# Optimization experiments

Hardware: AMD Instinct MI355X
Metric: run time of the kernel (lower is better)

Reference implementation:

```python
import jax, jax.numpy as jnp
import numpy as np

HEADS = 8
DIM_HEAD = 64
DIM = 256
INNER = HEADS * DIM_HEAD  # 512


def setup_inputs() -> dict:
    key = jax.random.key(0)
    ks = jax.random.split(key, 5)
    b_times_r, n = 32, 1024
    x = jax.random.normal(ks[0], (b_times_r, n, DIM), dtype=jnp.float32)
    # nn.Linear weights stored as (in, out) so y = x @ W
    Wq = jax.random.normal(ks[1], (DIM, INNER), dtype=jnp.float32) * 0.02
    Wkv = jax.random.normal(ks[2], (DIM, 2 * INNER), dtype=jnp.float32) * 0.02
    Wout = jax.random.normal(ks[3], (INNER, DIM), dtype=jnp.float32) * 0.02
    bout = jax.random.normal(ks[4], (DIM,), dtype=jnp.float32) * 0.02
    return {"x": x, "Wq": Wq, "Wkv": Wkv, "Wout": Wout, "bout": bout, "tie_attn_dim": 32}


def reference(x, Wq, Wkv, Wout, bout, tie_attn_dim):
    r = tie_attn_dim
    br, n, _ = x.shape
    b = br // r
    q = x @ Wq                                   # (b*r, n, inner)
    k, v = jnp.split(x @ Wkv, 2, axis=-1)        # (b*r, n, inner) each

    def split_heads(t):
        # (b*r) n (h d) -> b r h n d
        return t.reshape(b, r, n, HEADS, DIM_HEAD).transpose(0, 1, 3, 2, 4)

    q, k, v = map(split_heads, (q, k, v))
    scale = (DIM_HEAD ** -0.5) * (r ** -0.5)
    # tied attention: sum logits over the MSA row dim r
    dots = jnp.einsum('brhid,brhjd->bhij', q, k) * scale  # (b, h, n, n)
    attn = jax.nn.softmax(dots, axis=-1)
    out = jnp.einsum('bhij,brhjd->brhid', attn, v)        # (b, r, h, n, d)
    out = out.transpose(0, 1, 3, 2, 4).reshape(br, n, INNER)
    return out @ Wout + bout
```

## Files before the change

kernel.cpp:

```cpp
#include <hip/hip_runtime.h>
#include <math.h>

typedef unsigned short bf16u;
typedef __attribute__((ext_vector_type(8))) short short8;
typedef __attribute__((ext_vector_type(4))) float f32x4;

__device__ __forceinline__ bf16u f2bf(float f) {
    unsigned int u = __float_as_uint(f);
    u += 0x7fffu + ((u >> 16) & 1u);
    return (bf16u)(u >> 16);
}
__device__ __forceinline__ float bf2f(bf16u h) {
    return __uint_as_float(((unsigned int)h) << 16);
}

__device__ __forceinline__ void gload16(const void* g, void* s) {
    __builtin_amdgcn_global_load_lds((const __attribute__((address_space(1))) void*)g,
                                     (__attribute__((address_space(3))) void*)s, 16, 0, 0);
}

#define MM(a_, b_, c_) c_ = __builtin_amdgcn_mfma_f32_16x16x32_bf16(a_, b_, c_, 0, 0, 0)
#define BAR() __builtin_amdgcn_s_barrier()

#define STG() do { if (q < nht) { \
    const int t_ = q >> 2, p_ = q & 3; \
    const bf16u* P_ = (p_ < 2) ? B : A; \
    const long s_ = ((p_ < 2) ? brow : arow) + ((p_ & 1) ? r128 : 0) + t_ * 64; \
    bf16u* d_ = S + ((t_ & 1) << 15) + ((p_ < 2) ? 16384 : 0) + ((p_ & 1) << 12) + (w << 9); \
    gload16(P_ + s_, d_); \
    gload16(P_ + s_ + 32, d_ + 8192); \
  } ++q; } while (0)

#define RDA(dst, t, m, kk) dst = *(const short8*)(S + (((t) & 1) << 15) + ((kk) << 13) + ((wr * 8 + (m)) << 9) + (l << 3))
#define RDB(dst, t, n, kk) dst = *(const short8*)(S + (((t) & 1) << 15) + 16384 + ((kk) << 13) + ((wc * 4 + (n)) << 9) + (l << 3))

#define KTILE(t, VMASM) do { \
  RDA(af[0][0],t,0,0); RDA(af[0][1],t,0,1); RDA(af[1][0],t,1,0); RDA(af[1][1],t,1,1); \
  RDA(af[2][0],t,2,0); RDA(af[2][1],t,2,1); RDA(af[3][0],t,3,0); RDA(af[3][1],t,3,1); \
  RDB(b0[0][0],t,0,0); RDB(b0[0][1],t,0,1); RDB(b0[1][0],t,1,0); RDB(b0[1][1],t,1,1); \
  STG(); \
  BAR(); \
  __builtin_amdgcn_s_setprio(1); \
  MM(af[0][0],b0[0][0],acc[0][0]); MM(af[0][1],b0[0][1],acc[0][0]); \
  MM(af[0][0],b0[1][0],acc[0][1]); MM(af[0][1],b0[1][1],acc[0][1]); \
  MM(af[1][0],b0[0][0],acc[1][0]); MM(af[1][1],b0[0][1],acc[1][0]); \
  MM(af[1][0],b0[1][0],acc[1][1]); MM(af[1][1],b0[1][1],acc[1][1]); \
  MM(af[2][0],b0[0][0],acc[2][0]); MM(af[2][1],b0[0][1],acc[2][0]); \
  MM(af[2][0],b0[1][0],acc[2][1]); MM(af[2][1],b0[1][1],acc[2][1]); \
  MM(af[3][0],b0[0][0],acc[3][0]); MM(af[3][1],b0[0][1],acc[3][0]); \
  MM(af[3][0],b0[1][0],acc[3][1]); MM(af[3][1],b0[1][1],acc[3][1]); \
  __builtin_amdgcn_s_setprio(0); \
  BAR(); \
  RDB(b1[0][0],t,2,0); RDB(b1[0][1],t,2,1); RDB(b1[1][0],t,3,0); RDB(b1[1][1],t,3,1); \
  STG(); \
  BAR(); \
  __builtin_amdgcn_s_setprio(1); \
  MM(af[0][0],b1[0][0],acc[0][2]); MM(af[0][1],b1[0][1],acc[0][2]); \
  MM(af[0][0],b1[1][0],acc[0][3]); MM(af[0][1],b1[1][1],acc[0][3]); \
  MM(af[1][0],b1[0][0],acc[1][2]); MM(af[1][1],b1[0][1],acc[1][2]); \
  MM(af[1][0],b1[1][0],acc[1][3]); MM(af[1][1],b1[1][1],acc[1][3]); \
  MM(af[2][0],b1[0][0],acc[2][2]); MM(af[2][1],b1[0][1],acc[2][2]); \
  MM(af[2][0],b1[1][0],acc[2][3]); MM(af[2][1],b1[1][1],acc[2][3]); \
  MM(af[3][0],b1[0][0],acc[3][2]); MM(af[3][1],b1[0][1],acc[3][2]); \
  MM(af[3][0],b1[1][0],acc[3][3]); MM(af[3][1],b1[1][1],acc[3][3]); \
  __builtin_amdgcn_s_setprio(0); \
  BAR(); \
  RDA(af[0][0],t,4,0); RDA(af[0][1],t,4,1); RDA(af[1][0],t,5,0); RDA(af[1][1],t,5,1); \
  RDA(af[2][0],t,6,0); RDA(af[2][1],t,6,1); RDA(af[3][0],t,7,0); RDA(af[3][1],t,7,1); \
  STG(); \
  BAR(); \
  __builtin_amdgcn_s_setprio(1); \
  MM(af[0][0],b1[0][0],acc[4][2]); MM(af[0][1],b1[0][1],acc[4][2]); \
  MM(af[0][0],b1[1][0],acc[4][3]); MM(af[0][1],b1[1][1],acc[4][3]); \
  MM(af[1][0],b1[0][0],acc[5][2]); MM(af[1][1],b1[0][1],acc[5][2]); \
  MM(af[1][0],b1[1][0],acc[5][3]); MM(af[1][1],b1[1][1],acc[5][3]); \
  MM(af[2][0],b1[0][0],acc[6][2]); MM(af[2][1],b1[0][1],acc[6][2]); \
  MM(af[2][0],b1[1][0],acc[6][3]); MM(af[2][1],b1[1][1],acc[6][3]); \
  MM(af[3][0],b1[0][0],acc[7][2]); MM(af[3][1],b1[0][1],acc[7][2]); \
  MM(af[3][0],b1[1][0],acc[7][3]); MM(af[3][1],b1[1][1],acc[7][3]); \
  __builtin_amdgcn_s_setprio(0); \
  BAR(); \
  STG(); \
  BAR(); \
  __builtin_amdgcn_s_setprio(1); \
  MM(af[0][0],b0[0][0],acc[4][0]); MM(af[0][1],b0[0][1],acc[4][0]); \
  MM(af[0][0],b0[1][0],acc[4][1]); MM(af[0][1],b0[1][1],acc[4][1]); \
  MM(af[1][0],b0[0][0],acc[5][0]); MM(af[1][1],b0[0][1],acc[5][0]); \
  MM(af[1][0],b0[1][0],acc[5][1]); MM(af[1][1],b0[1][1],acc[5][1]); \
  MM(af[2][0],b0[0][0],acc[6][0]); MM(af[2][1],b0[0][1],acc[6][0]); \
  MM(af[2][0],b0[1][0],acc[6][1]); MM(af[2][1],b0[1][1],acc[6][1]); \
  MM(af[3][0],b0[0][0],acc[7][0]); MM(af[3][1],b0[0][1],acc[7][0]); \
  MM(af[3][0],b0[1][0],acc[7][1]); MM(af[3][1],b0[1][1],acc[7][1]); \
  __builtin_amdgcn_s_setprio(0); \
  VMASM; \
  BAR(); \
} while (0)

template<int EPI>
__global__ __launch_bounds__(512, 2) void gemm8(
    const bf16u* __restrict__ Aall, const bf16u* __restrict__ Ball,
    int Kld, int Kloop, long splitOff, long sAz, long sBz,
    bf16u* __restrict__ D0, bf16u* __restrict__ D1, bf16u* __restrict__ D2,
    float scale)
{
    const int gx = gridDim.x, gy = gridDim.y;
    const int nwg = gx * gy * gridDim.z;
    int flat = blockIdx.x + gx * (blockIdx.y + gy * blockIdx.z);
    int swz = (nwg & 7) ? flat : (flat & 7) * (nwg >> 3) + (flat >> 3);
    const int bx = swz % gx;
    int tq = swz / gx;
    const int by = tq % gy;
    const int z = tq / gy;

    const int tid = threadIdx.x;
    const int l = tid & 63, w = tid >> 6;
    const int fr = l & 15, fq = l >> 4;
    const int wr = w >> 2, wc = w & 3;
    const bf16u* A = Aall + (long)(z & 7) * sAz + (long)(z >> 3) * splitOff;
    const bf16u* B = Ball + (long)(z & 7) * sBz + (long)(z >> 3) * splitOff;
    const int m0 = by << 8, n0 = bx << 8;

    __shared__ __align__(16) bf16u S[65536];

    f32x4 acc[8][4];
#pragma unroll
    for (int i = 0; i < 8; ++i)
#pragma unroll
        for (int j = 0; j < 4; ++j) acc[i][j] = (f32x4){0.f, 0.f, 0.f, 0.f};

    const int NT = Kloop >> 6;
    const int nht = NT << 2;
    const int NI = NT >> 1;
    int q = 0;

    const long arow = (long)(m0 + w * 16 + fr) * Kld + fq * 8;
    const long brow = (long)(n0 + w * 16 + fr) * Kld + fq * 8;
    const long r128 = (long)128 * Kld;

    STG(); STG(); STG(); STG(); STG(); STG();
    asm volatile("s_waitcnt vmcnt(4)" ::: "memory");
    BAR();

    short8 af[4][2], b0[2][2], b1[2][2];

    for (int i = 0; i < NI - 1; ++i) {
        KTILE(2 * i,     asm volatile("s_waitcnt vmcnt(4)" ::: "memory"));
        KTILE(2 * i + 1, asm volatile("s_waitcnt vmcnt(4)" ::: "memory"));
    }
    KTILE(2 * NI - 2, asm volatile("s_waitcnt vmcnt(0)" ::: "memory"));
    KTILE(2 * NI - 1, (void)0);

    const int colb = n0 + wc * 64;
    const int rowb = m0 + wr * 128;
    if constexpr (EPI == 1) {
        const int rr = m0 >> 10, i0 = m0 & 1023;
        if (n0 >= 1024) {
            const int c2 = n0 - 1024;
#pragma unroll
            for (int pv = 0; pv < 2; ++pv) {
                __syncthreads();
                if ((wc >> 1) == pv) {
#pragma unroll
                    for (int m = 0; m < 8; ++m)
#pragma unroll
                        for (int n = 0; n < 4; ++n) {
                            const int cl = (wc & 1) * 64 + n * 16 + fr;
                            const int rowl = wr * 128 + m * 16 + fq * 4;
                            ushort4 pk;
                            pk.x = f2bf(acc[m][n][0]); pk.y = f2bf(acc[m][n][1]);
                            pk.z = f2bf(acc[m][n][2]); pk.w = f2bf(acc[m][n][3]);
                            *(ushort4*)(S + cl * 264 + rowl) = pk;
                        }
                }
                __syncthreads();
#pragma unroll
                for (int p = 0; p < 8; ++p) {
                    const int idx = p * 512 + tid;
                    const int ch = idx >> 5;
                    const int c8 = (idx & 31) * 8;
                    const int col = c2 + pv * 128 + ch;
                    const int h = col >> 6, d = col & 63;
                    *(short8*)(D2 + ((long)(h * 2048 + rr * 64 + d) << 10) + i0 + c8)
                        = *(const short8*)(S + ch * 264 + c8);
                }
            }
        } else {
            bf16u* Dqk = (n0 < 512) ? D0 : D1;
            const int nq = (n0 < 512) ? n0 : n0 - 512;
#pragma unroll
            for (int p2 = 0; p2 < 2; ++p2) {
                __syncthreads();
                if (wr == p2) {
#pragma unroll
                    for (int m = 0; m < 8; ++m)
#pragma unroll
                        for (int n = 0; n < 4; ++n) {
                            const int cl = wc * 64 + n * 16 + fr;
                            const int rl = m * 16 + fq * 4;
#pragma unroll
                            for (int r = 0; r < 4; ++r)
                                S[(rl + r) * 264 + cl] = f2bf(acc[m][n][r]);
                        }
                }
                __syncthreads();
#pragma unroll
                for (int p = 0; p < 8; ++p) {
                    const int idx = p * 512 + tid;
                    const int row = idx >> 5;
                    const int col = (idx & 31) * 8;
                    const int h = (nq + col) >> 6, d0 = (nq + col) & 63;
                    const int il = p2 * 128 + row;
                    *(short8*)(Dqk + ((long)(h * 1024 + i0 + il) << 11) + rr * 64 + d0)
                        = *(const short8*)(S + row * 264 + col);
                }
            }
        }
    } else if constexpr (EPI == 2) {
#pragma unroll
        for (int m = 0; m < 8; ++m)
#pragma unroll
            for (int n = 0; n < 4; ++n) {
                const int col = colb + n * 16 + fr;
                const int rb = rowb + m * 16 + fq * 4;
#pragma unroll
                for (int r = 0; r < 4; ++r)
                    D0[((long)z << 20) + ((long)(rb + r) << 10) + col] = f2bf(acc[m][n][r] * scale);
            }
    } else {
#pragma unroll
        for (int m = 0; m < 8; ++m)
#pragma unroll
            for (int n = 0; n < 4; ++n) {
                const int col = colb + n * 16 + fr;
                const int cb = col >> 6, d = col & 63;
                const int rb = rowb + m * 16 + fq * 4;
#pragma unroll
                for (int r = 0; r < 4; ++r)
                    D0[((long)(cb * 1024 + rb + r) << 9) + (z & 7) * 64 + d] = f2bf(acc[m][n][r]);
            }
    }
}

__global__ __launch_bounds__(256, 4) void gemm_out(
    const bf16u* __restrict__ A, const bf16u* __restrict__ B, int K,
    float* __restrict__ Df, const float* __restrict__ bias)
{
    const int gx = gridDim.x, gy = gridDim.y;
    const int nwg = gx * gy;
    int flat = blockIdx.x + gx * blockIdx.y;
    int swz = (nwg & 7) ? flat : (flat & 7) * (nwg >> 3) + (flat >> 3);
    const int bx = swz % gx, by = swz / gx;

    const int tid = threadIdx.x;
    const int l = tid & 63, w = tid >> 6;
    const int fr = l & 15, fq = l >> 4;
    const int kb = fq * 8;
    const int m0 = by * 128, n0 = bx * 128;

    __shared__ __align__(16) bf16u S[16896];

    f32x4 acc[4][4];
#pragma unroll
    for (int i = 0; i < 4; ++i)
#pragma unroll
        for (int j = 0; j < 4; ++j) acc[i][j] = (f32x4){0.f, 0.f, 0.f, 0.f};

    const long aoff0 = (long)(m0 + w * 16 + fr) * K + kb;
    const long aoff1 = (long)(m0 + (w + 4) * 16 + fr) * K + kb;
    const long boff0 = (long)(n0 + w * 16 + fr) * K + kb;
    const long boff1 = (long)(n0 + (w + 4) * 16 + fr) * K + kb;

    const int wr = w >> 1, wc = w & 1;

#define STAGE(c, k0) do { \
        bf16u* as_ = S + (c) * 4096; \
        bf16u* bs_ = S + 8192 + (c) * 4096; \
        gload16(A + aoff0 + (k0), as_ + w * 512); \
        gload16(A + aoff1 + (k0), as_ + w * 512 + 2048); \
        gload16(B + boff0 + (k0), bs_ + w * 512); \
        gload16(B + boff1 + (k0), bs_ + w * 512 + 2048); \
    } while (0)

    STAGE(0, 0);
    __syncthreads();

    int cur = 0;
    for (int k0 = 0; k0 < K; k0 += 32) {
        if (k0 + 32 < K) STAGE(cur ^ 1, k0 + 32);

        const bf16u* Ac = S + cur * 4096;
        const bf16u* Bc = S + 8192 + cur * 4096;
        short8 af[4], bg[4];
#pragma unroll
        for (int t = 0; t < 4; ++t) {
            af[t] = *(const short8*)(Ac + (wr * 4 + t) * 512 + l * 8);
            bg[t] = *(const short8*)(Bc + (wc * 4 + t) * 512 + l * 8);
        }
#pragma unroll
        for (int mt = 0; mt < 4; ++mt)
#pragma unroll
            for (int nt = 0; nt < 4; ++nt)
                acc[mt][nt] = __builtin_amdgcn_mfma_f32_16x16x32_bf16(
                    af[mt], bg[nt], acc[mt][nt], 0, 0, 0);
        __syncthreads();
        cur ^= 1;
    }
#undef STAGE

    float* Sf = (float*)S;
#pragma unroll
    for (int p2 = 0; p2 < 2; ++p2) {
        __syncthreads();
        if (wr == p2) {
#pragma unroll
            for (int mt = 0; mt < 4; ++mt)
#pragma unroll
                for (int nt = 0; nt < 4; ++nt) {
                    const int cl = wc * 64 + nt * 16 + fr;
                    const float b = bias[n0 + cl];
                    const int rl = mt * 16 + fq * 4;
#pragma unroll
                    for (int r = 0; r < 4; ++r)
                        Sf[(rl + r) * 132 + cl] = acc[mt][nt][r] + b;
                }
        }
        __syncthreads();
#pragma unroll
        for (int p = 0; p < 8; ++p) {
            const int idx = p * 256 + tid;
            const int row = idx >> 5;
            const int c4 = (idx & 31) * 4;
            const float4 v = *(const float4*)(Sf + row * 132 + c4);
            *(float4*)(Df + (long)(m0 + p2 * 64 + row) * 256 + n0 + c4) = v;
        }
    }
}

__global__ __launch_bounds__(256) void cvt_x(const float* __restrict__ in,
                                             bf16u* __restrict__ out) {
    const long idx = (long)(blockIdx.x * 256 + threadIdx.x) * 4;
    const float4 v = *(const float4*)(in + idx);
    ushort4 o;
    o.x = f2bf(v.x); o.y = f2bf(v.y); o.z = f2bf(v.z); o.w = f2bf(v.w);
    *(ushort4*)(out + idx) = o;
}

__global__ __launch_bounds__(256) void transpose_cvt(const float* __restrict__ in,
                                                     bf16u* __restrict__ out,
                                                     int R, int C) {
    const int idx = blockIdx.x * 256 + threadIdx.x;
    if (idx < R * C) {
        const int r = idx / C, c = idx % C;
        out[(long)c * R + r] = f2bf(in[idx]);
    }
}

__global__ __launch_bounds__(256) void softmax_rows2(const bf16u* __restrict__ attP,
                                                     bf16u* __restrict__ att) {
    const long base = (long)blockIdx.x << 10;
    const int tid = threadIdx.x;
    const uint2 u0 = *(const uint2*)(attP + base + tid * 4);
    const uint2 u1 = *(const uint2*)(attP + 8388608 + base + tid * 4);
    const float v0 = bf2f(u0.x & 0xffffu) + bf2f(u1.x & 0xffffu);
    const float v1 = bf2f(u0.x >> 16)     + bf2f(u1.x >> 16);
    const float v2 = bf2f(u0.y & 0xffffu) + bf2f(u1.y & 0xffffu);
    const float v3 = bf2f(u0.y >> 16)     + bf2f(u1.y >> 16);
    float m = fmaxf(fmaxf(v0, v1), fmaxf(v2, v3));
#pragma unroll
    for (int o = 32; o; o >>= 1) m = fmaxf(m, __shfl_xor(m, o));
    __shared__ float red[8];
    if ((tid & 63) == 0) red[tid >> 6] = m;
    __syncthreads();
    m = fmaxf(fmaxf(red[0], red[1]), fmaxf(red[2], red[3]));
    const float e0 = __expf(v0 - m), e1 = __expf(v1 - m);
    const float e2 = __expf(v2 - m), e3 = __expf(v3 - m);
    float s = e0 + e1 + e2 + e3;
#pragma unroll
    for (int o = 32; o; o >>= 1) s += __shfl_xor(s, o);
    if ((tid & 63) == 0) red[4 + (tid >> 6)] = s;
    __syncthreads();
    const float inv = 1.0f / (red[4] + red[5] + red[6] + red[7]);
    uint2 o2;
    o2.x = (unsigned)f2bf(e0 * inv) | ((unsigned)f2bf(e1 * inv) << 16);
    o2.y = (unsigned)f2bf(e2 * inv) | ((unsigned)f2bf(e3 * inv) << 16);
    *(uint2*)(att + base + tid * 4) = o2;
}

extern "C" void kernel_launch(void* const* d_in, const int* in_sizes, int n_in,
                              void* d_out, int out_size, void* d_ws, size_t ws_size,
                              hipStream_t stream) {
    (void)in_sizes; (void)n_in; (void)out_size; (void)ws_size;
    const float* x    = (const float*)d_in[0];
    const float* Wq   = (const float*)d_in[1];
    const float* Wkv  = (const float*)d_in[2];
    const float* Wout = (const float*)d_in[3];
    const float* bout = (const float*)d_in[4];
    float* out = (float*)d_out;

    char* ws = (char*)d_ws;
    bf16u* xb    = (bf16u*)(ws);
    bf16u* WqkvT = (bf16u*)(ws + 16777216);
    bf16u* WoutT = (bf16u*)(ws + 17563648);
    bf16u* Qt    = (bf16u*)(ws + 17825792);
    bf16u* Kt    = (bf16u*)(ws + 51380224);
    bf16u* Vt2   = (bf16u*)(ws + 84934656);
    bf16u* att   = (bf16u*)(ws + 118489088);
    bf16u* out2  = (bf16u*)(ws + 135266304);
    bf16u* attP  = out2;

    cvt_x<<<8192, 256, 0, stream>>>(x, xb);
    transpose_cvt<<<512, 256, 0, stream>>>(Wq, WqkvT, 256, 512);
    transpose_cvt<<<1024, 256, 0, stream>>>(Wkv, WqkvT + 512 * 256, 256, 1024);
    transpose_cvt<<<512, 256, 0, stream>>>(Wout, WoutT, 512, 256);

    const float scale = 1.0f / (8.0f * sqrtf(32.0f));

    gemm8<1><<<dim3(6, 128, 1), 512, 0, stream>>>(
        xb, WqkvT, 256, 256, 0, 0, 0, Qt, Kt, Vt2, 0.f);

    gemm8<2><<<dim3(4, 4, 16), 512, 0, stream>>>(
        Qt, Kt, 2048, 1024, 1024, 1024L * 2048, 1024L * 2048, attP, nullptr, nullptr, scale);

    softmax_rows2<<<8192, 256, 0, stream>>>(attP, att);

    gemm8<3><<<dim3(8, 4, 8), 512, 0, stream>>>(
        att, Vt2, 1024, 1024, 0, 1024L * 1024, 2048L * 1024, out2, nullptr, nullptr, 0.f);

    gemm_out<<<dim3(2, 256, 1), 256, 0, stream>>>(
        out2, WoutT, 512, out, bout);
}
```

Baseline: 255.3 us.

## Use r-major Q/K layout and stage GEMM epilogues through LDS for coalesced stores

Q and K are now stored as (h, r, i, d) blocks with 64-element rows instead of interleaving r inside a 2048-wide row, and the GEMM loader gets separate row and K-tile strides so each 64-wide K tile comes from a different r slab. The logits and attention-times-V epilogues now stage bf16 results through shared memory and write 16-byte vectors, replacing scattered 2-byte stores. The goal is to cut uncoalesced global writes in the QK^T and AV epilogues. In exchange it adds extra barriers and LDS round trips, and the K-tile loads now jump between strided slabs.

```diff
diff --git a/kernel.cpp b/kernel.cpp
--- a/kernel.cpp
+++ b/kernel.cpp
@@ -25,7 +25,8 @@
 #define STG() do { if (q < nht) { \
     const int t_ = q >> 2, p_ = q & 3; \
     const bf16u* P_ = (p_ < 2) ? B : A; \
-    const long s_ = ((p_ < 2) ? brow : arow) + ((p_ & 1) ? r128 : 0) + t_ * 64; \
+    const long s_ = (p_ < 2) ? (brow + ((p_ & 1) ? r128b : 0) + (long)t_ * tsB) \
+                             : (arow + ((p_ & 1) ? r128a : 0) + (long)t_ * tsA); \
     bf16u* d_ = S + ((t_ & 1) << 15) + ((p_ < 2) ? 16384 : 0) + ((p_ & 1) << 12) + (w << 9); \
     gload16(P_ + s_, d_); \
     gload16(P_ + s_ + 32, d_ + 8192); \
@@ -96,10 +97,26 @@
   BAR(); \
 } while (0)
 
+#define EPISTAGE(P2, SCL) do { \
+    if (wr == (P2)) { \
+        _Pragma("unroll") \
+        for (int m = 0; m < 8; ++m) \
+            _Pragma("unroll") \
+            for (int n = 0; n < 4; ++n) { \
+                const int cl = wc * 64 + n * 16 + fr; \
+                const int rl = m * 16 + fq * 4; \
+                _Pragma("unroll") \
+                for (int r = 0; r < 4; ++r) \
+                    S[(rl + r) * 264 + cl] = f2bf(acc[m][n][r] * (SCL)); \
+            } \
+    } \
+} while (0)
+
 template<int EPI>
 __global__ __launch_bounds__(512, 2) void gemm8(
     const bf16u* __restrict__ Aall, const bf16u* __restrict__ Ball,
-    int Kld, int Kloop, long splitOff, long sAz, long sBz,
+    int RSa, int RSb, long tsA, long tsB, int Kloop,
+    long splitOff, long sAz, long sBz,
     bf16u* __restrict__ D0, bf16u* __restrict__ D1, bf16u* __restrict__ D2,
     float scale)
 {
@@ -133,9 +150,10 @@
     const int NI = NT >> 1;
     int q = 0;
 
-    const long arow = (long)(m0 + w * 16 + fr) * Kld + fq * 8;
-    const long brow = (long)(n0 + w * 16 + fr) * Kld + fq * 8;
-    const long r128 = (long)128 * Kld;
+    const long arow = (long)(m0 + w * 16 + fr) * RSa + fq * 8;
+    const long brow = (long)(n0 + w * 16 + fr) * RSb + fq * 8;
+    const long r128a = (long)128 * RSa;
+    const long r128b = (long)128 * RSb;
 
     STG(); STG(); STG(); STG(); STG(); STG();
     asm volatile("s_waitcnt vmcnt(4)" ::: "memory");
@@ -150,8 +168,6 @@
     KTILE(2 * NI - 2, asm volatile("s_waitcnt vmcnt(0)" ::: "memory"));
     KTILE(2 * NI - 1, (void)0);
 
-    const int colb = n0 + wc * 64;
-    const int rowb = m0 + wr * 128;
     if constexpr (EPI == 1) {
         const int rr = m0 >> 10, i0 = m0 & 1023;
         if (n0 >= 1024) {
@@ -190,54 +206,54 @@
 #pragma unroll
             for (int p2 = 0; p2 < 2; ++p2) {
                 __syncthreads();
-                if (wr == p2) {
-#pragma unroll
-                    for (int m = 0; m < 8; ++m)
-#pragma unroll
-                        for (int n = 0; n < 4; ++n) {
-                            const int cl = wc * 64 + n * 16 + fr;
-                            const int rl = m * 16 + fq * 4;
-#pragma unroll
-                            for (int r = 0; r < 4; ++r)
-                                S[(rl + r) * 264 + cl] = f2bf(acc[m][n][r]);
-                        }
-                }
+                EPISTAGE(p2, 1.0f);
                 __syncthreads();
 #pragma unroll
                 for (int p = 0; p < 8; ++p) {
                     const int idx = p * 512 + tid;
                     const int row = idx >> 5;
-                    const int col = (idx & 31) * 8;
-                    const int h = (nq + col) >> 6, d0 = (nq + col) & 63;
+                    const int c = (idx & 31) * 8;
+                    const int h = (nq + c) >> 6, d0 = (nq + c) & 63;
                     const int il = p2 * 128 + row;
-                    *(short8*)(Dqk + ((long)(h * 1024 + i0 + il) << 11) + rr * 64 + d0)
-                        = *(const short8*)(S + row * 264 + col);
+                    *(short8*)(Dqk + (long)h * 2097152 + (long)rr * 65536
+                               + (long)(i0 + il) * 64 + d0)
+                        = *(const short8*)(S + row * 264 + c);
                 }
             }
         }
     } else if constexpr (EPI == 2) {
 #pragma unroll
-        for (int m = 0; m < 8; ++m)
-#pragma unroll
-            for (int n = 0; n < 4; ++n) {
-                const int col = colb + n * 16 + fr;
-                const int rb = rowb + m * 16 + fq * 4;
-#pragma unroll
-                for (int r = 0; r < 4; ++r)
-                    D0[((long)z << 20) + ((long)(rb + r) << 10) + col] = f2bf(acc[m][n][r] * scale);
+        for (int p2 = 0; p2 < 2; ++p2) {
+            __syncthreads();
+            EPISTAGE(p2, scale);
+            __syncthreads();
+#pragma unroll
+            for (int p = 0; p < 8; ++p) {
+                const int idx = p * 512 + tid;
+                const int row = idx >> 5;
+                const int c = (idx & 31) * 8;
+                *(short8*)(D0 + ((long)z << 20)
+                           + ((long)(m0 + p2 * 128 + row) << 10) + n0 + c)
+                    = *(const short8*)(S + row * 264 + c);
             }
+        }
     } else {
 #pragma unroll
-        for (int m = 0; m < 8; ++m)
-#pragma unroll
-            for (int n = 0; n < 4; ++n) {
-                const int col = colb + n * 16 + fr;
-                const int cb = col >> 6, d = col & 63;
-                const int rb = rowb + m * 16 + fq * 4;
-#pragma unroll
-                for (int r = 0; r < 4; ++r)
-                    D0[((long)(cb * 1024 + rb + r) << 9) + (z & 7) * 64 + d] = f2bf(acc[m][n][r]);
+        for (int p2 = 0; p2 < 2; ++p2) {
+            __syncthreads();
+            EPISTAGE(p2, 1.0f);
+            __syncthreads();
+#pragma unroll
+            for (int p = 0; p < 8; ++p) {
+                const int idx = p * 512 + tid;
+                const int row = idx >> 5;
+                const int c = (idx & 31) * 8;
+                const int rr = (n0 + c) >> 6, d0 = (n0 + c) & 63;
+                const int i = m0 + p2 * 128 + row;
+                *(short8*)(D0 + (((long)(rr * 1024 + i)) << 9) + (z & 7) * 64 + d0)
+                    = *(const short8*)(S + row * 264 + c);
             }
+        }
     }
 }
 
@@ -416,15 +432,17 @@
     const float scale = 1.0f / (8.0f * sqrtf(32.0f));
 
     gemm8<1><<<dim3(6, 128, 1), 512, 0, stream>>>(
-        xb, WqkvT, 256, 256, 0, 0, 0, Qt, Kt, Vt2, 0.f);
+        xb, WqkvT, 256, 256, 64, 64, 256, 0, 0, 0, Qt, Kt, Vt2, 0.f);
 
     gemm8<2><<<dim3(4, 4, 16), 512, 0, stream>>>(
-        Qt, Kt, 2048, 1024, 1024, 1024L * 2048, 1024L * 2048, attP, nullptr, nullptr, scale);
+        Qt, Kt, 64, 64, 65536, 65536, 1024, 1048576, 2097152, 2097152,
+        attP, nullptr, nullptr, scale);
 
     softmax_rows2<<<8192, 256, 0, stream>>>(attP, att);
 
     gemm8<3><<<dim3(8, 4, 8), 512, 0, stream>>>(
-        att, Vt2, 1024, 1024, 0, 1024L * 1024, 2048L * 1024, out2, nullptr, nullptr, 0.f);
+        att, Vt2, 1024, 1024, 64, 64, 1024, 0, 1048576, 2097152,
+        out2, nullptr, nullptr, 0.f);
 
     gemm_out<<<dim3(2, 256, 1), 256, 0, stream>>>(
         out2, WoutT, 512, out, bout);
```

Measured after the change: 255.8 us. About the same (+0.2%).
